# Kernel tuning notes

Hardware: AMD Instinct MI355X
Metric: run time of the kernel (lower is better)

Reference implementation:

```python
import jax, jax.numpy as jnp
import numpy as np

N = 20000
D = 64


def gcn_conv(x, src, dst, ew, W, b, n_nodes):
    # PyG GCNConv: lin -> gcn_norm (with self loops) -> scatter-add -> +bias
    loop = jnp.arange(n_nodes)
    s = jnp.concatenate([src, loop])
    d = jnp.concatenate([dst, loop])
    w = jnp.concatenate([ew, jnp.ones((n_nodes,), ew.dtype)])
    deg = jax.ops.segment_sum(w, d, num_segments=n_nodes)
    dinv = jnp.where(deg > 0, jax.lax.rsqrt(deg), 0.0)
    norm = dinv[s] * w * dinv[d]  # [E+N]
    h = x @ W  # [N, D]
    msg = h[s] * norm[:, None]  # gather + scale
    out = jax.ops.segment_sum(msg, d, num_segments=n_nodes)  # scatter-add
    return out + b


def layernorm(x, gamma, beta, eps=1e-5):
    mu = jnp.mean(x, axis=-1, keepdims=True)
    var = jnp.var(x, axis=-1, keepdims=True)
    return (x - mu) * jax.lax.rsqrt(var + eps) * gamma + beta


def setup_inputs() -> dict:
    key = jax.random.key(0)
    ks = jax.random.split(key, 12)
    E = 640000
    x = jax.random.normal(ks[0], (N, D), jnp.float32)
    edge_index = jax.random.randint(ks[1], (2, E), 0, N, jnp.int64)
    edge_weight = jax.random.uniform(ks[2], (E,), jnp.float32)
    glorot = 1.0 / np.sqrt(D)
    Wc1 = jax.random.uniform(ks[3], (D, D), jnp.float32, -glorot, glorot)
    bc1 = jnp.zeros((D,), jnp.float32)
    Wc2 = jax.random.uniform(ks[4], (D, D), jnp.float32, -glorot, glorot)
    bc2 = jnp.zeros((D,), jnp.float32)
    # xavier_uniform on (num_labels*D, D) view: bound = sqrt(6/(D+D))
    bnd = np.sqrt(6.0 / (2 * D))
    W1 = jax.random.uniform(ks[5], (N, D, D), jnp.float32, -bnd, bnd)
    b1 = jnp.zeros((N, D), jnp.float32)
    W2 = jax.random.uniform(ks[6], (N, D, D), jnp.float32, -bnd, bnd)
    b2 = jnp.zeros((N, D), jnp.float32)
    ln_gamma = jnp.ones((D,), jnp.float32)
    ln_beta = jnp.zeros((D,), jnp.float32)
    return {"x": x, "edge_index": edge_index, "edge_weight": edge_weight,
            "Wc1": Wc1, "bc1": bc1, "Wc2": Wc2, "bc2": bc2,
            "W1": W1, "b1": b1, "W2": W2, "b2": b2,
            "ln_gamma": ln_gamma, "ln_beta": ln_beta}


def reference(x, edge_index, edge_weight, Wc1, bc1, Wc2, bc2, W1, b1, W2, b2, ln_gamma, ln_beta):
    src, dst = edge_index[0], edge_index[1]
    h = gcn_conv(x, src, dst, edge_weight, Wc1, bc1, N)
    h = jax.nn.selu(h)
    h = gcn_conv(h, src, dst, edge_weight, Wc2, bc2, N)
    h = jax.nn.selu(h)
    # per-node label-specific transform (num_labels == N)
    t = jnp.einsum('nd,ndj->nj', h, W1) + b1
    t = layernorm(t, ln_gamma, ln_beta)
    t = jnp.einsum('nd,ndj->nj', t, W2) + b2
    return t
```

## Files before the change

kernel.cpp:

```cpp
#include <hip/hip_runtime.h>
#include <stdint.h>

#define ND 64

typedef __attribute__((ext_vector_type(4))) float floatx4;
typedef __attribute__((ext_vector_type(4))) short shortx4;
typedef __attribute__((ext_vector_type(8))) short short8;

__device__ __forceinline__ float bf2f(unsigned short u) {
  union { unsigned int i; float f; } v; v.i = ((unsigned int)u) << 16; return v.f;
}
__device__ __forceinline__ unsigned short f2bf(float f) {
  union { float f; unsigned int i; } v; v.f = f;
  unsigned int x = v.i;
  return (unsigned short)((x + 0x7fffu + ((x >> 16) & 1u)) >> 16);
}
__device__ __forceinline__ float selu_f(float x) {
  float r = x > 0.f ? x : 1.6732632423543772f * expm1f(x);
  return 1.0507009873554805f * r;
}
__device__ __forceinline__ bool is_bf16_data(const void* gam) {
  return ((const unsigned short*)gam)[0] == 0x3F80;
}
__device__ __forceinline__ float ldE(const void* p, size_t i, bool bf) {
  return bf ? bf2f(((const unsigned short*)p)[i]) : ((const float*)p)[i];
}
__device__ __forceinline__ floatx4 ld4(const void* p, size_t i, bool bf) {
  floatx4 r;
  if (bf) {
    shortx4 v = *(const shortx4*)((const unsigned short*)p + i);
#pragma unroll
    for (int k = 0; k < 4; ++k) r[k] = bf2f((unsigned short)v[k]);
  } else {
    r = *(const floatx4*)((const float*)p + i);
  }
  return r;
}

__global__ void k_pre(float* deg, int* cnt, int n) {
  int i = blockIdx.x * blockDim.x + threadIdx.x;
  if (i < n) { deg[i] = 1.0f; cnt[i] = 0; }
}

__global__ void k_deg(const int* __restrict__ dst, const void* __restrict__ ew,
                      float* deg, int* cnt, int E, const void* __restrict__ gam) {
  bool bf = is_bf16_data(gam);
  int e = blockIdx.x * blockDim.x + threadIdx.x;
  if (e < E) {
    int d = dst[e];
    atomicAdd(&deg[d], ldE(ew, e, bf));
    atomicAdd(&cnt[d], 1);
  }
}

__global__ __launch_bounds__(1024) void k_scan(const int* __restrict__ cnt,
                                               const float* __restrict__ deg, float* dinv,
                                               int* row_ptr, int* cursor, int n) {
  __shared__ int part[1024];
  int t = threadIdx.x;
  int C = (n + 1023) >> 10;
  int base = t * C;
  for (int k = 0; k < C; ++k) {
    int i = base + k;
    if (i < n) { float g = deg[i]; dinv[i] = g > 0.f ? rsqrtf(g) : 0.f; }
  }
  int s = 0;
  for (int k = 0; k < C; ++k) { int i = base + k; if (i < n) s += cnt[i]; }
  part[t] = s;
  __syncthreads();
  for (int off = 1; off < 1024; off <<= 1) {
    int v = (t >= off) ? part[t - off] : 0;
    __syncthreads();
    if (t >= off) part[t] += v;
    __syncthreads();
  }
  int run = (t == 0) ? 0 : part[t - 1];
  for (int k = 0; k < C; ++k) {
    int i = base + k;
    if (i < n) { row_ptr[i] = run; cursor[i] = run; run += cnt[i]; }
  }
  if (t == 1023) row_ptr[n] = part[1023];
}

__global__ void k_fill(const int* __restrict__ src, const int* __restrict__ dst,
                       const void* __restrict__ ew, const float* __restrict__ dinv,
                       int* cursor, int* csr_src, float* csr_norm, int E,
                       const void* __restrict__ gam) {
  bool bf = is_bf16_data(gam);
  int e = blockIdx.x * blockDim.x + threadIdx.x;
  if (e < E) {
    int s = src[e], d = dst[e];
    int pos = atomicAdd(&cursor[d], 1);
    csr_src[pos] = s;
    csr_norm[pos] = dinv[s] * ldE(ew, e, bf) * dinv[d];
  }
}

template <int IN_EXT>
__global__ __launch_bounds__(256) void k_gemm(const void* __restrict__ X,
                                              const void* __restrict__ Wc,
                                              float* __restrict__ H, int n,
                                              const void* __restrict__ gam) {
  bool bf = is_bf16_data(gam);
  int lane = threadIdx.x & 63;
  int jg = lane & 15, dg = lane >> 4;
  float w[16][4];
#pragma unroll
  for (int dd = 0; dd < 16; ++dd) {
    floatx4 v = ld4(Wc, (size_t)(dd * 4 + dg) * 64 + jg * 4, bf);
#pragma unroll
    for (int k = 0; k < 4; ++k) w[dd][k] = v[k];
  }
  int wave = (blockIdx.x * blockDim.x + threadIdx.x) >> 6;
  int nw = (gridDim.x * blockDim.x) >> 6;
  for (int nn = wave; nn < n; nn += nw) {
    float hreg = IN_EXT ? ldE(X, (size_t)nn * 64 + lane, bf)
                        : ((const float*)X)[(size_t)nn * 64 + lane];
    float acc[4] = {0.f, 0.f, 0.f, 0.f};
#pragma unroll
    for (int dd = 0; dd < 16; ++dd) {
      float hv = __shfl(hreg, dd * 4 + dg);
#pragma unroll
      for (int k = 0; k < 4; ++k) acc[k] += hv * w[dd][k];
    }
#pragma unroll
    for (int k = 0; k < 4; ++k) acc[k] += __shfl_xor(acc[k], 16);
#pragma unroll
    for (int k = 0; k < 4; ++k) acc[k] += __shfl_xor(acc[k], 32);
    if (lane < 16) {
      floatx4 o = {acc[0], acc[1], acc[2], acc[3]};
      *(floatx4*)(H + (size_t)nn * 64 + lane * 4) = o;
    }
  }
}

__global__ __launch_bounds__(256) void k_agg(const float* __restrict__ h,
                                             const int* __restrict__ row_ptr,
                                             const int* __restrict__ csr_src,
                                             const float* __restrict__ csr_norm,
                                             const float* __restrict__ dinv,
                                             const void* __restrict__ bias,
                                             float* __restrict__ outp, int n,
                                             const void* __restrict__ gam) {
  bool bf = is_bf16_data(gam);
  int wv = (blockIdx.x * blockDim.x + threadIdx.x) >> 6;
  int lane = threadIdx.x & 63;
  if (wv >= n) return;
  float di = dinv[wv];
  float acc = di * di * h[(size_t)wv * 64 + lane];
  int k = row_ptr[wv], end = row_ptr[wv + 1];
  while (k < end) {
    int cnt = end - k;
    if (cnt > 64) cnt = 64;
    int ms = 0; float mw = 0.f;
    if (lane < cnt) { ms = csr_src[k + lane]; mw = csr_norm[k + lane]; }
    for (int j = 0; j < cnt; ++j) {
      int s = __shfl(ms, j);
      float w = __shfl(mw, j);
      acc += w * h[(size_t)s * 64 + lane];
    }
    k += cnt;
  }
  acc += ldE(bias, lane, bf);
  outp[(size_t)wv * 64 + lane] = selu_f(acc);
}

__global__ __launch_bounds__(256) void k_fused(const float* __restrict__ g2,
                                               const void* __restrict__ W1,
                                               const void* __restrict__ b1,
                                               const void* __restrict__ W2,
                                               const void* __restrict__ b2,
                                               const void* __restrict__ gam,
                                               const void* __restrict__ bet,
                                               void* __restrict__ out, int n) {
  __shared__ float tbuf[4][64];
  bool bf = is_bf16_data(gam);
  int wid = threadIdx.x >> 6;
  int lane = threadIdx.x & 63;
  int nn = blockIdx.x * 4 + wid;
  if (nn >= n) nn = n - 1;
  float hreg = g2[(size_t)nn * 64 + lane];
  size_t Wb = (size_t)nn * 4096;

  if (bf) {
    int jg = lane & 7, dg = lane >> 3;
    int j0 = jg * 8;
    const unsigned short* W1p = (const unsigned short*)W1 + Wb;
    const unsigned short* W2p = (const unsigned short*)W2 + Wb;
    float acc[8];
#pragma unroll
    for (int k = 0; k < 8; ++k) acc[k] = 0.f;
#pragma unroll
    for (int dd = 0; dd < 8; ++dd) {
      int d = dd * 8 + dg;
      float hv = __shfl(hreg, d);
      short8 w = *(const short8*)(W1p + d * 64 + j0);
#pragma unroll
      for (int k = 0; k < 8; ++k) acc[k] += hv * bf2f((unsigned short)w[k]);
    }
#pragma unroll
    for (int m = 8; m <= 32; m <<= 1)
#pragma unroll
      for (int k = 0; k < 8; ++k) acc[k] += __shfl_xor(acc[k], m);
    short8 bb = *(const short8*)((const unsigned short*)b1 + (size_t)nn * 64 + j0);
#pragma unroll
    for (int k = 0; k < 8; ++k) acc[k] += bf2f((unsigned short)bb[k]);

    float s1 = 0.f, s2 = 0.f;
#pragma unroll
    for (int k = 0; k < 8; ++k) { s1 += acc[k]; s2 += acc[k] * acc[k]; }
#pragma unroll
    for (int m = 1; m <= 4; m <<= 1) { s1 += __shfl_xor(s1, m); s2 += __shfl_xor(s2, m); }
    float mean = s1 * (1.f / 64.f);
    float var = s2 * (1.f / 64.f) - mean * mean;
    if (var < 0.f) var = 0.f;
    float rinv = rsqrtf(var + 1e-5f);
    short8 gm = *(const short8*)((const unsigned short*)gam + j0);
    short8 bt = *(const short8*)((const unsigned short*)bet + j0);
    float tn[8];
#pragma unroll
    for (int k = 0; k < 8; ++k)
      tn[k] = (acc[k] - mean) * rinv * bf2f((unsigned short)gm[k]) + bf2f((unsigned short)bt[k]);
    if (lane < 8) {
#pragma unroll
      for (int k = 0; k < 8; ++k) tbuf[wid][lane * 8 + k] = tn[k];
    }
    __syncthreads();

    float acc2[8];
#pragma unroll
    for (int k = 0; k < 8; ++k) acc2[k] = 0.f;
#pragma unroll
    for (int dd = 0; dd < 8; ++dd) {
      int d = dd * 8 + dg;
      float tv = tbuf[wid][d];
      short8 w = *(const short8*)(W2p + d * 64 + j0);
#pragma unroll
      for (int k = 0; k < 8; ++k) acc2[k] += tv * bf2f((unsigned short)w[k]);
    }
#pragma unroll
    for (int m = 8; m <= 32; m <<= 1)
#pragma unroll
      for (int k = 0; k < 8; ++k) acc2[k] += __shfl_xor(acc2[k], m);
    short8 b2v = *(const short8*)((const unsigned short*)b2 + (size_t)nn * 64 + j0);
#pragma unroll
    for (int k = 0; k < 8; ++k) acc2[k] += bf2f((unsigned short)b2v[k]);
    if (lane < 8) {
      short8 o;
#pragma unroll
      for (int k = 0; k < 8; ++k) o[k] = (short)f2bf(acc2[k]);
      *(short8*)((unsigned short*)out + (size_t)nn * 64 + lane * 8) = o;
    }
  } else {
    int jg = lane & 15, dg = lane >> 4;
    int j0 = jg * 4;
    const float* W1p = (const float*)W1 + Wb;
    const float* W2p = (const float*)W2 + Wb;
    float acc[4] = {0.f, 0.f, 0.f, 0.f};
#pragma unroll
    for (int dd = 0; dd < 16; ++dd) {
      int d = dd * 4 + dg;
      float hv = __shfl(hreg, d);
      floatx4 w = *(const floatx4*)(W1p + d * 64 + j0);
#pragma unroll
      for (int k = 0; k < 4; ++k) acc[k] += hv * w[k];
    }
#pragma unroll
    for (int m = 16; m <= 32; m <<= 1)
#pragma unroll
      for (int k = 0; k < 4; ++k) acc[k] += __shfl_xor(acc[k], m);
    floatx4 bb = *(const floatx4*)((const float*)b1 + (size_t)nn * 64 + j0);
#pragma unroll
    for (int k = 0; k < 4; ++k) acc[k] += bb[k];

    float s1 = 0.f, s2 = 0.f;
#pragma unroll
    for (int k = 0; k < 4; ++k) { s1 += acc[k]; s2 += acc[k] * acc[k]; }
#pragma unroll
    for (int m = 1; m <= 8; m <<= 1) { s1 += __shfl_xor(s1, m); s2 += __shfl_xor(s2, m); }
    float mean = s1 * (1.f / 64.f);
    float var = s2 * (1.f / 64.f) - mean * mean;
    if (var < 0.f) var = 0.f;
    float rinv = rsqrtf(var + 1e-5f);
    floatx4 gm = *(const floatx4*)((const float*)gam + j0);
    floatx4 bt = *(const floatx4*)((const float*)bet + j0);
    float tn[4];
#pragma unroll
    for (int k = 0; k < 4; ++k) tn[k] = (acc[k] - mean) * rinv * gm[k] + bt[k];
    if (lane < 16) {
#pragma unroll
      for (int k = 0; k < 4; ++k) tbuf[wid][lane * 4 + k] = tn[k];
    }
    __syncthreads();

    float acc2[4] = {0.f, 0.f, 0.f, 0.f};
#pragma unroll
    for (int dd = 0; dd < 16; ++dd) {
      int d = dd * 4 + dg;
      float tv = tbuf[wid][d];
      floatx4 w = *(const floatx4*)(W2p + d * 64 + j0);
#pragma unroll
      for (int k = 0; k < 4; ++k) acc2[k] += tv * w[k];
    }
#pragma unroll
    for (int m = 16; m <= 32; m <<= 1)
#pragma unroll
      for (int k = 0; k < 4; ++k) acc2[k] += __shfl_xor(acc2[k], m);
    floatx4 b2v = *(const floatx4*)((const float*)b2 + (size_t)nn * 64 + j0);
#pragma unroll
    for (int k = 0; k < 4; ++k) acc2[k] += b2v[k];
    if (lane < 16) {
      floatx4 o = {acc2[0], acc2[1], acc2[2], acc2[3]};
      *(floatx4*)((float*)out + (size_t)nn * 64 + lane * 4) = o;
    }
  }
}

extern "C" void kernel_launch(void* const* d_in, const int* in_sizes, int n_in,
                              void* d_out, int out_size, void* d_ws, size_t ws_size,
                              hipStream_t stream) {
  const int N = in_sizes[0] / ND;
  const int E = in_sizes[2];
  const void* x   = d_in[0];
  const int* ei   = (const int*)d_in[1];
  const void* ew  = d_in[2];
  const void* Wc1 = d_in[3];
  const void* bc1 = d_in[4];
  const void* Wc2 = d_in[5];
  const void* bc2 = d_in[6];
  const void* W1  = d_in[7];
  const void* b1  = d_in[8];
  const void* W2  = d_in[9];
  const void* b2  = d_in[10];
  const void* gam = d_in[11];
  const void* bet = d_in[12];
  const int* srcp = ei;
  const int* dstp = ei + E;

  char* ws = (char*)d_ws;
  size_t off = 0;
  auto take = [&](size_t bytes) {
    void* p = ws + off;
    off = (off + bytes + 255) & ~(size_t)255;
    return p;
  };
  float* deg      = (float*)take((size_t)N * 4);
  float* dinv     = (float*)take((size_t)N * 4);
  int* cnt        = (int*)take((size_t)N * 4);
  int* row_ptr    = (int*)take((size_t)(N + 1) * 4);
  int* cursor     = (int*)take((size_t)N * 4);
  int* csr_src    = (int*)take((size_t)E * 4);
  float* csr_norm = (float*)take((size_t)E * 4);
  float* h        = (float*)take((size_t)N * ND * 4);
  float* g1       = (float*)take((size_t)N * ND * 4);
  float* g2       = (float*)take((size_t)N * ND * 4);
  (void)ws_size; (void)n_in; (void)out_size;

  k_pre<<<(N + 255) / 256, 256, 0, stream>>>(deg, cnt, N);
  k_deg<<<(E + 255) / 256, 256, 0, stream>>>(dstp, ew, deg, cnt, E, gam);
  k_scan<<<1, 1024, 0, stream>>>(cnt, deg, dinv, row_ptr, cursor, N);
  k_fill<<<(E + 255) / 256, 256, 0, stream>>>(srcp, dstp, ew, dinv, cursor, csr_src, csr_norm, E, gam);
  k_gemm<1><<<256, 256, 0, stream>>>(x, Wc1, h, N, gam);
  k_agg<<<(N + 3) / 4, 256, 0, stream>>>(h, row_ptr, csr_src, csr_norm, dinv, bc1, g1, N, gam);
  k_gemm<0><<<256, 256, 0, stream>>>(g1, Wc2, h, N, gam);
  k_agg<<<(N + 3) / 4, 256, 0, stream>>>(h, row_ptr, csr_src, csr_norm, dinv, bc2, g2, N, gam);
  k_fused<<<(N + 3) / 4, 256, 0, stream>>>(g2, W1, b1, W2, b2, gam, bet, d_out, N);
}
```

Measured before the change: 912.1 us.

## Pack CSR and degree data into u64, store GEMM output as bf16, unroll gather

Degree and in-edge count are packed into one 64-bit fixed-point atomic, and the scan is staged in LDS. CSR source index and normalisation are packed into a single u64 per edge. The intermediate GEMM output is stored as bf16 to halve random gather traffic, and the aggregation loop uses four independent accumulators to keep more loads in flight. The cost is reduced precision from bf16 features and fixed-point degrees.

```diff
diff --git a/kernel.cpp b/kernel.cpp
--- a/kernel.cpp
+++ b/kernel.cpp
@@ -6,6 +6,7 @@
 typedef __attribute__((ext_vector_type(4))) float floatx4;
 typedef __attribute__((ext_vector_type(4))) short shortx4;
 typedef __attribute__((ext_vector_type(8))) short short8;
+typedef unsigned long long u64;
 
 __device__ __forceinline__ float bf2f(unsigned short u) {
   union { unsigned int i; float f; } v; v.i = ((unsigned int)u) << 16; return v.f;
@@ -37,35 +38,41 @@
   return r;
 }
 
-__global__ void k_pre(float* deg, int* cnt, int n) {
+__global__ void k_pre(u64* packed, int n) {
   int i = blockIdx.x * blockDim.x + threadIdx.x;
-  if (i < n) { deg[i] = 1.0f; cnt[i] = 0; }
+  if (i < n) packed[i] = 16777216ULL;
 }
 
 __global__ void k_deg(const int* __restrict__ dst, const void* __restrict__ ew,
-                      float* deg, int* cnt, int E, const void* __restrict__ gam) {
+                      u64* packed, int E, const void* __restrict__ gam) {
   bool bf = is_bf16_data(gam);
   int e = blockIdx.x * blockDim.x + threadIdx.x;
   if (e < E) {
-    int d = dst[e];
-    atomicAdd(&deg[d], ldE(ew, e, bf));
-    atomicAdd(&cnt[d], 1);
-  }
-}
-
-__global__ __launch_bounds__(1024) void k_scan(const int* __restrict__ cnt,
-                                               const float* __restrict__ deg, float* dinv,
-                                               int* row_ptr, int* cursor, int n) {
+    float w = ldE(ew, e, bf);
+    u64 a = (1ULL << 48) | (u64)(long long)(w * 16777216.0f + 0.5f);
+    atomicAdd(&packed[dst[e]], a);
+  }
+}
+
+__global__ __launch_bounds__(1024) void k_scan(const u64* __restrict__ packed,
+                                               float* __restrict__ dinv,
+                                               int* __restrict__ row_ptr,
+                                               int* __restrict__ cursor, int n) {
+  extern __shared__ int lds[];
   __shared__ int part[1024];
   int t = threadIdx.x;
+  for (int i = t; i < n; i += 1024) {
+    u64 p = packed[i];
+    lds[i] = (int)(p >> 48);
+    float g = (float)(p & 0xFFFFFFFFFFFFULL) * 5.9604644775390625e-8f;
+    dinv[i] = g > 0.f ? rsqrtf(g) : 0.f;
+  }
+  __syncthreads();
   int C = (n + 1023) >> 10;
   int base = t * C;
-  for (int k = 0; k < C; ++k) {
-    int i = base + k;
-    if (i < n) { float g = deg[i]; dinv[i] = g > 0.f ? rsqrtf(g) : 0.f; }
-  }
+  int lim = base + C; if (lim > n) lim = n;
   int s = 0;
-  for (int k = 0; k < C; ++k) { int i = base + k; if (i < n) s += cnt[i]; }
+  for (int i = base; i < lim; ++i) s += lds[i];
   part[t] = s;
   __syncthreads();
   for (int off = 1; off < 1024; off <<= 1) {
@@ -75,31 +82,30 @@
     __syncthreads();
   }
   int run = (t == 0) ? 0 : part[t - 1];
-  for (int k = 0; k < C; ++k) {
-    int i = base + k;
-    if (i < n) { row_ptr[i] = run; cursor[i] = run; run += cnt[i]; }
-  }
-  if (t == 1023) row_ptr[n] = part[1023];
+  for (int i = base; i < lim; ++i) { int c = lds[i]; lds[i] = run; run += c; }
+  __syncthreads();
+  for (int i = t; i < n; i += 1024) { int v = lds[i]; row_ptr[i] = v; cursor[i] = v; }
+  if (t == 0) row_ptr[n] = part[1023];
 }
 
 __global__ void k_fill(const int* __restrict__ src, const int* __restrict__ dst,
                        const void* __restrict__ ew, const float* __restrict__ dinv,
-                       int* cursor, int* csr_src, float* csr_norm, int E,
+                       int* cursor, u64* __restrict__ csr, int E,
                        const void* __restrict__ gam) {
   bool bf = is_bf16_data(gam);
   int e = blockIdx.x * blockDim.x + threadIdx.x;
   if (e < E) {
     int s = src[e], d = dst[e];
+    float nm = dinv[s] * ldE(ew, e, bf) * dinv[d];
     int pos = atomicAdd(&cursor[d], 1);
-    csr_src[pos] = s;
-    csr_norm[pos] = dinv[s] * ldE(ew, e, bf) * dinv[d];
+    csr[pos] = ((u64)__float_as_uint(nm) << 32) | (unsigned int)s;
   }
 }
 
 template <int IN_EXT>
 __global__ __launch_bounds__(256) void k_gemm(const void* __restrict__ X,
                                               const void* __restrict__ Wc,
-                                              float* __restrict__ H, int n,
+                                              unsigned short* __restrict__ H, int n,
                                               const void* __restrict__ gam) {
   bool bf = is_bf16_data(gam);
   int lane = threadIdx.x & 63;
@@ -128,16 +134,17 @@
 #pragma unroll
     for (int k = 0; k < 4; ++k) acc[k] += __shfl_xor(acc[k], 32);
     if (lane < 16) {
-      floatx4 o = {acc[0], acc[1], acc[2], acc[3]};
-      *(floatx4*)(H + (size_t)nn * 64 + lane * 4) = o;
-    }
-  }
-}
-
-__global__ __launch_bounds__(256) void k_agg(const float* __restrict__ h,
+      shortx4 o;
+#pragma unroll
+      for (int k = 0; k < 4; ++k) o[k] = (short)f2bf(acc[k]);
+      *(shortx4*)(H + (size_t)nn * 64 + lane * 4) = o;
+    }
+  }
+}
+
+__global__ __launch_bounds__(256) void k_agg(const unsigned short* __restrict__ h,
                                              const int* __restrict__ row_ptr,
-                                             const int* __restrict__ csr_src,
-                                             const float* __restrict__ csr_norm,
+                                             const u64* __restrict__ csr,
                                              const float* __restrict__ dinv,
                                              const void* __restrict__ bias,
                                              float* __restrict__ outp, int n,
@@ -147,21 +154,35 @@
   int lane = threadIdx.x & 63;
   if (wv >= n) return;
   float di = dinv[wv];
-  float acc = di * di * h[(size_t)wv * 64 + lane];
+  float a0 = di * di * bf2f(h[(size_t)wv * 64 + lane]);
+  float a1 = 0.f, a2 = 0.f, a3 = 0.f;
   int k = row_ptr[wv], end = row_ptr[wv + 1];
   while (k < end) {
     int cnt = end - k;
     if (cnt > 64) cnt = 64;
-    int ms = 0; float mw = 0.f;
-    if (lane < cnt) { ms = csr_src[k + lane]; mw = csr_norm[k + lane]; }
-    for (int j = 0; j < cnt; ++j) {
-      int s = __shfl(ms, j);
-      float w = __shfl(mw, j);
-      acc += w * h[(size_t)s * 64 + lane];
+    u64 mv = 0;
+    if (lane < cnt) mv = csr[k + lane];
+    int j = 0;
+    for (; j + 4 <= cnt; j += 4) {
+      u64 v0 = __shfl(mv, j), v1 = __shfl(mv, j + 1);
+      u64 v2 = __shfl(mv, j + 2), v3 = __shfl(mv, j + 3);
+      float h0 = bf2f(h[(size_t)(unsigned int)(v0 & 0xFFFFFFFFu) * 64 + lane]);
+      float h1 = bf2f(h[(size_t)(unsigned int)(v1 & 0xFFFFFFFFu) * 64 + lane]);
+      float h2 = bf2f(h[(size_t)(unsigned int)(v2 & 0xFFFFFFFFu) * 64 + lane]);
+      float h3 = bf2f(h[(size_t)(unsigned int)(v3 & 0xFFFFFFFFu) * 64 + lane]);
+      a0 += __uint_as_float((unsigned int)(v0 >> 32)) * h0;
+      a1 += __uint_as_float((unsigned int)(v1 >> 32)) * h1;
+      a2 += __uint_as_float((unsigned int)(v2 >> 32)) * h2;
+      a3 += __uint_as_float((unsigned int)(v3 >> 32)) * h3;
+    }
+    for (; j < cnt; ++j) {
+      u64 v = __shfl(mv, j);
+      a0 += __uint_as_float((unsigned int)(v >> 32)) *
+            bf2f(h[(size_t)(unsigned int)(v & 0xFFFFFFFFu) * 64 + lane]);
     }
     k += cnt;
   }
-  acc += ldE(bias, lane, bf);
+  float acc = (a0 + a1) + (a2 + a3) + ldE(bias, lane, bf);
   outp[(size_t)wv * 64 + lane] = selu_f(acc);
 }
 
@@ -344,25 +365,23 @@
     off = (off + bytes + 255) & ~(size_t)255;
     return p;
   };
-  float* deg      = (float*)take((size_t)N * 4);
+  u64* packed     = (u64*)take((size_t)N * 8);
   float* dinv     = (float*)take((size_t)N * 4);
-  int* cnt        = (int*)take((size_t)N * 4);
   int* row_ptr    = (int*)take((size_t)(N + 1) * 4);
   int* cursor     = (int*)take((size_t)N * 4);
-  int* csr_src    = (int*)take((size_t)E * 4);
-  float* csr_norm = (float*)take((size_t)E * 4);
-  float* h        = (float*)take((size_t)N * ND * 4);
+  u64* csr        = (u64*)take((size_t)E * 8);
+  unsigned short* h = (unsigned short*)take((size_t)N * ND * 2);
   float* g1       = (float*)take((size_t)N * ND * 4);
   float* g2       = (float*)take((size_t)N * ND * 4);
   (void)ws_size; (void)n_in; (void)out_size;
 
-  k_pre<<<(N + 255) / 256, 256, 0, stream>>>(deg, cnt, N);
-  k_deg<<<(E + 255) / 256, 256, 0, stream>>>(dstp, ew, deg, cnt, E, gam);
-  k_scan<<<1, 1024, 0, stream>>>(cnt, deg, dinv, row_ptr, cursor, N);
-  k_fill<<<(E + 255) / 256, 256, 0, stream>>>(srcp, dstp, ew, dinv, cursor, csr_src, csr_norm, E, gam);
+  k_pre<<<(N + 255) / 256, 256, 0, stream>>>(packed, N);
+  k_deg<<<(E + 255) / 256, 256, 0, stream>>>(dstp, ew, packed, E, gam);
+  k_scan<<<1, 1024, (size_t)N * 4, stream>>>(packed, dinv, row_ptr, cursor, N);
+  k_fill<<<(E + 255) / 256, 256, 0, stream>>>(srcp, dstp, ew, dinv, cursor, csr, E, gam);
   k_gemm<1><<<256, 256, 0, stream>>>(x, Wc1, h, N, gam);
-  k_agg<<<(N + 3) / 4, 256, 0, stream>>>(h, row_ptr, csr_src, csr_norm, dinv, bc1, g1, N, gam);
+  k_agg<<<(N + 3) / 4, 256, 0, stream>>>(h, row_ptr, csr, dinv, bc1, g1, N, gam);
   k_gemm<0><<<256, 256, 0, stream>>>(g1, Wc2, h, N, gam);
-  k_agg<<<(N + 3) / 4, 256, 0, stream>>>(h, row_ptr, csr_src, csr_norm, dinv, bc2, g2, N, gam);
+  k_agg<<<(N + 3) / 4, 256, 0, stream>>>(h, row_ptr, csr, dinv, bc2, g2, N, gam);
   k_fused<<<(N + 3) / 4, 256, 0, stream>>>(g2, W1, b1, W2, b2, gam, bet, d_out, N);
 }
```

After: 782.6 us. -14.2%, faster.
